# Performance work log

Measured on AMD Instinct MI355X. Metric: run time of the kernel, lower is better.

The kernel has to match this reference:

```python
import jax, jax.numpy as jnp
import numpy as np

B, T, D = 2, 2048, 1024
H, d = 16, 64
INNER = H * d
K = 4  # conv_size
EPS_RMS = 1e-6
EPS_NORM = 1e-12


def _dconv(x, w, b):
    # depthwise causal conv: x (B,T,C), w (C,K), b (C,)
    xp = jnp.pad(x, ((0, 0), (K - 1, 0), (0, 0)))
    Tt = x.shape[1]
    out = b
    for k in range(K):
        out = out + xp[:, k:k + Tt] * w[:, k]
    return out


def _l2norm(x):
    n = jnp.sqrt(jnp.sum(x * x, axis=-1, keepdims=True))
    return x / jnp.maximum(n, EPS_NORM)


def setup_inputs() -> dict:
    key = jax.random.key(0)
    ks = jax.random.split(key, 12)
    s = 0.02
    inp = {
        'x': jax.random.normal(ks[0], (B, T, D), jnp.float32),
        'Wq': jax.random.normal(ks[1], (D, INNER), jnp.float32) * s,
        'Wk': jax.random.normal(ks[2], (D, INNER), jnp.float32) * s,
        'Wv': jax.random.normal(ks[3], (D, INNER), jnp.float32) * s,
        'Wa': jax.random.normal(ks[4], (D, H), jnp.float32) * s,
        'ba': jnp.full((H,), 2.0, jnp.float32),
        'Wb': jax.random.normal(ks[5], (D, H), jnp.float32) * s,
        'bb': jnp.zeros((H,), jnp.float32),
        'Wg': jax.random.normal(ks[6], (D, INNER), jnp.float32) * s,
        'Wo': jax.random.normal(ks[7], (INNER, D), jnp.float32) * s,
        'cq_w': jax.random.normal(ks[8], (INNER, K), jnp.float32) * 0.3,
        'cq_b': jnp.zeros((INNER,), jnp.float32),
        'ck_w': jax.random.normal(ks[9], (INNER, K), jnp.float32) * 0.3,
        'ck_b': jnp.zeros((INNER,), jnp.float32),
        'cv_w': jax.random.normal(ks[10], (INNER, K), jnp.float32) * 0.3,
        'cv_b': jnp.zeros((INNER,), jnp.float32),
        'gamma': jnp.zeros((INNER,), jnp.float32),
    }
    return inp


def reference(x, Wq, Wk, Wv, Wa, ba, Wb, bb, Wg, Wo,
              cq_w, cq_b, ck_w, ck_b, cv_w, cv_b, gamma):
    q = jax.nn.silu(_dconv(x @ Wq, cq_w, cq_b))
    k = jax.nn.silu(_dconv(x @ Wk, ck_w, ck_b))
    v = jax.nn.silu(_dconv(x @ Wv, cv_w, cv_b))
    q = _l2norm(q.reshape(B, T, H, d))
    k = _l2norm(k.reshape(B, T, H, d))
    v = v.reshape(B, T, H, d)
    alpha = jax.nn.sigmoid(x @ Wa + ba)  # (B,T,H)
    beta = jax.nn.sigmoid(x @ Wb + bb)   # (B,T,H)
    gate = jax.nn.silu(x @ Wg)           # (B,T,INNER)

    I_d = jnp.eye(d, dtype=x.dtype)

    def step(S, ins):
        q_t, k_t, v_t, a_t, b_t = ins  # q/k/v: (B,H,d); a,b: (B,H)
        a = a_t[..., None, None]
        b = b_t[..., None, None]
        kkT = k_t[..., :, None] * k_t[..., None, :]   # (B,H,d,d)
        vkT = v_t[..., :, None] * k_t[..., None, :]
        decay = a * (I_d - b * kkT)
        S = jnp.matmul(S, decay) + b * vkT
        o = jnp.einsum('bhde,bhe->bhd', S, q_t)
        return S, o

    # time-major scan inputs
    qT = jnp.transpose(q, (1, 0, 2, 3))
    kT = jnp.transpose(k, (1, 0, 2, 3))
    vT = jnp.transpose(v, (1, 0, 2, 3))
    aT = jnp.transpose(alpha, (1, 0, 2))
    bT = jnp.transpose(beta, (1, 0, 2))
    S0 = jnp.zeros((B, H, d, d), x.dtype)
    _, oT = jax.lax.scan(step, S0, (qT, kT, vT, aT, bT))  # (T,B,H,d)

    out = jnp.transpose(oT, (1, 0, 2, 3)).reshape(B, T, INNER)
    rms = jnp.sqrt(jnp.mean(out * out, axis=-1, keepdims=True) + EPS_RMS)
    out = out / rms * (1.0 + gamma)
    out = out * gate
    return out @ Wo
```

## Files before the change

### kernel.cpp

```cpp
#include <hip/hip_runtime.h>
#include <hip/hip_bf16.h>
#include <cmath>

#define B_ 2
#define T_ 2048
#define D_ 1024
#define H_ 16
#define DH 64
#define INNER_ 1024
#define BT (B_*T_)
#define NCH 32
#define NU (B_*H_*NCH)

typedef __attribute__((ext_vector_type(8))) __bf16 bf16x8;
typedef __attribute__((ext_vector_type(4))) float f32x4;
typedef const __attribute__((address_space(1))) unsigned gas_u32;
typedef __attribute__((address_space(3))) unsigned las_u32;

__device__ __forceinline__ void async16(const void* g, void* l) {
  __builtin_amdgcn_global_load_lds((gas_u32*)g, (las_u32*)l, 16, 0, 0);
}

__device__ __forceinline__ ushort bfr(float x) {
  __hip_bfloat16 t = __float2bfloat16(x);
  return *(ushort*)&t;
}
__device__ __forceinline__ void st_bf4(__hip_bfloat16* p, float a, float b, float c, float d) {
  ushort4 u; u.x = bfr(a); u.y = bfr(b); u.z = bfr(c); u.w = bfr(d);
  *(ushort4*)p = u;
}

__global__ __launch_bounds__(256) void cvt_bf16_kernel(const float* __restrict__ in,
                                                       __hip_bfloat16* __restrict__ out,
                                                       int n4) {
  int i = blockIdx.x * 256 + threadIdx.x;
  if (i >= n4) return;
  float4 v = *(const float4*)(in + (size_t)i * 4);
  __hip_bfloat16 t[4];
  t[0] = __float2bfloat16(v.x); t[1] = __float2bfloat16(v.y);
  t[2] = __float2bfloat16(v.z); t[3] = __float2bfloat16(v.w);
  *(uint2*)(out + (size_t)i * 4) = *(uint2*)t;
}

__global__ __launch_bounds__(256) void transpose_cvt_kernel(const float* __restrict__ in,
                                                            __hip_bfloat16* __restrict__ out,
                                                            int R, int C) {
  __shared__ float tile[32][33];
  const int bc = blockIdx.x * 32, br = blockIdx.y * 32;
  const int tx = threadIdx.x & 31, ty = threadIdx.x >> 5;
#pragma unroll
  for (int i = 0; i < 32; i += 8)
    tile[ty + i][tx] = in[(size_t)(br + ty + i) * C + bc + tx];
  __syncthreads();
#pragma unroll
  for (int i = 0; i < 32; i += 8)
    out[(size_t)(bc + ty + i) * R + br + tx] = __float2bfloat16(tile[tx][ty + i]);
}

__global__ __launch_bounds__(256) void wab_kernel(const float* __restrict__ Wa,
                                                  const float* __restrict__ Wb,
                                                  __hip_bfloat16* __restrict__ Wabt) {
  int idx = blockIdx.x * 256 + threadIdx.x;
  int j = idx >> 10, k = idx & 1023;
  float v = 0.f;
  if (j < 16) v = Wa[k * 16 + j];
  else if (j < 32) v = Wb[k * 16 + (j - 16)];
  Wabt[idx] = __float2bfloat16(v);
}

__global__ __launch_bounds__(256) void gemm_bf16(const __hip_bfloat16* __restrict__ A,
                                                 const __hip_bfloat16* __restrict__ Bt,
                                                 float* __restrict__ C,
                                                 int M, int N, int K, int act) {
  __shared__ __hip_bfloat16 As[128 * 32];
  __shared__ __hip_bfloat16 Bs[128 * 32];
  const int tid = threadIdx.x;
  const int lane = tid & 63, wave = tid >> 6;
  const int wr = wave >> 1, wc = wave & 1;
  const int m0 = blockIdx.y * 128, n0 = blockIdx.x * 128;
  const int srow = tid >> 2, skoff = (tid & 3) * 8;
  const int l15 = lane & 15, lg = lane >> 4;

  f32x4 acc[4][4];
#pragma unroll
  for (int m = 0; m < 4; ++m)
#pragma unroll
    for (int n = 0; n < 4; ++n) acc[m][n] = (f32x4)0.f;

  char* asB = (char*)As;
  char* bsB = (char*)Bs;
  const int ldsw = wave * 1024;

  for (int k0 = 0; k0 < K; k0 += 32) {
    async16(A + (size_t)(m0 + srow) * K + k0 + skoff, asB + ldsw);
    async16(A + (size_t)(m0 + 64 + srow) * K + k0 + skoff, asB + 4096 + ldsw);
    async16(Bt + (size_t)(n0 + srow) * K + k0 + skoff, bsB + ldsw);
    async16(Bt + (size_t)(n0 + 64 + srow) * K + k0 + skoff, bsB + 4096 + ldsw);
    __syncthreads();

    bf16x8 af[4], bfg[4];
#pragma unroll
    for (int m = 0; m < 4; ++m)
      af[m] = *(const bf16x8*)(asB + ((wr * 64 + m * 16 + l15) * 32 + lg * 8) * 2);
#pragma unroll
    for (int n = 0; n < 4; ++n)
      bfg[n] = *(const bf16x8*)(bsB + ((wc * 64 + n * 16 + l15) * 32 + lg * 8) * 2);
#pragma unroll
    for (int m = 0; m < 4; ++m)
#pragma unroll
      for (int n = 0; n < 4; ++n)
        acc[m][n] = __builtin_amdgcn_mfma_f32_16x16x32_bf16(af[m], bfg[n], acc[m][n], 0, 0, 0);
    __syncthreads();
  }

#pragma unroll
  for (int m = 0; m < 4; ++m) {
    const int rbase = m0 + wr * 64 + m * 16 + lg * 4;
#pragma unroll
    for (int n = 0; n < 4; ++n) {
      const int col = n0 + wc * 64 + n * 16 + l15;
#pragma unroll
      for (int r = 0; r < 4; ++r) {
        float vv = acc[m][n][r];
        if (act == 1) vv = vv / (1.f + expf(-vv));
        C[(size_t)(rbase + r) * N + col] = vv;
      }
    }
  }
}

__global__ __launch_bounds__(256) void gemm_ab(const __hip_bfloat16* __restrict__ A,
                                               const __hip_bfloat16* __restrict__ Bt,
                                               const float* __restrict__ ba,
                                               const float* __restrict__ bb2,
                                               float* __restrict__ alpha,
                                               float* __restrict__ beta, int K) {
  __shared__ __hip_bfloat16 As[128 * 32];
  __shared__ __hip_bfloat16 Bs[128 * 32];
  const int tid = threadIdx.x;
  const int lane = tid & 63, wave = tid >> 6;
  const int wr = wave >> 1, wc = wave & 1;
  const int m0 = blockIdx.y * 128;
  const int srow = tid >> 2, skoff = (tid & 3) * 8;
  const int l15 = lane & 15, lg = lane >> 4;

  f32x4 acc[4][2];
#pragma unroll
  for (int m = 0; m < 4; ++m)
#pragma unroll
    for (int n = 0; n < 2; ++n) acc[m][n] = (f32x4)0.f;

  char* asB = (char*)As;
  char* bsB = (char*)Bs;
  const int ldsw = wave * 1024;

  for (int k0 = 0; k0 < K; k0 += 32) {
    async16(A + (size_t)(m0 + srow) * K + k0 + skoff, asB + ldsw);
    async16(A + (size_t)(m0 + 64 + srow) * K + k0 + skoff, asB + 4096 + ldsw);
    async16(Bt + (size_t)srow * K + k0 + skoff, bsB + ldsw);
    async16(Bt + (size_t)(64 + srow) * K + k0 + skoff, bsB + 4096 + ldsw);
    __syncthreads();
    if (wc == 0) {
      bf16x8 af[4], bfg[2];
#pragma unroll
      for (int m = 0; m < 4; ++m)
        af[m] = *(const bf16x8*)(asB + ((wr * 64 + m * 16 + l15) * 32 + lg * 8) * 2);
#pragma unroll
      for (int n = 0; n < 2; ++n)
        bfg[n] = *(const bf16x8*)(bsB + ((n * 16 + l15) * 32 + lg * 8) * 2);
#pragma unroll
      for (int m = 0; m < 4; ++m)
#pragma unroll
        for (int n = 0; n < 2; ++n)
          acc[m][n] = __builtin_amdgcn_mfma_f32_16x16x32_bf16(af[m], bfg[n], acc[m][n], 0, 0, 0);
    }
    __syncthreads();
  }
  if (wc != 0) return;
#pragma unroll
  for (int m = 0; m < 4; ++m) {
    const int rbase = m0 + wr * 64 + m * 16 + lg * 4;
#pragma unroll
    for (int n = 0; n < 2; ++n) {
      const int col = n * 16 + l15;
      const float bias = (n == 0) ? ba[l15] : bb2[l15];
      float* dst = (n == 0) ? alpha : beta;
#pragma unroll
      for (int r = 0; r < 4; ++r) {
        float vv = acc[m][n][r] + bias;
        dst[(size_t)(rbase + r) * H_ + l15] = 1.f / (1.f + expf(-vv));
      }
    }
  }
}

__device__ __forceinline__ bf16x8 pfrag(const __hip_bfloat16* buf, int row, int ks, int lg) {
  return *(const bf16x8*)((const char*)buf + row * 128 + ks * 64 + lg * 16);
}

__global__ __launch_bounds__(512, 2) void gemm256(const __hip_bfloat16* __restrict__ A,
                                                  const __hip_bfloat16* __restrict__ Bt,
                                                  float* __restrict__ C,
                                                  int M, int N, int K, int act) {
  __shared__ __hip_bfloat16 As[2][256 * 64];
  __shared__ __hip_bfloat16 Bs[2][256 * 64];
  const int tid = threadIdx.x;
  const int lane = tid & 63, wv = tid >> 6;
  const int wr = wv >> 2, wc = wv & 3;
  const int m0 = blockIdx.y * 256, n0 = blockIdx.x * 256;
  const int l15 = lane & 15, lg = lane >> 4;
  const int sr8 = lane >> 3, sc = (lane & 7) * 8;

  f32x4 acc[8][4];
#pragma unroll
  for (int m = 0; m < 8; ++m)
#pragma unroll
    for (int n = 0; n < 4; ++n) acc[m][n] = (f32x4)0.f;

  auto stage = [&](int kt, int bsel) {
    const size_t k0 = (size_t)kt * 64;
    const __hip_bfloat16* Ab = A + (size_t)(m0 + wv * 8 + sr8) * K + k0 + sc;
    const __hip_bfloat16* Bb = Bt + (size_t)(n0 + wv * 8 + sr8) * K + k0 + sc;
    char* al = (char*)As[bsel] + wv * 1024;
    char* bl = (char*)Bs[bsel] + wv * 1024;
#pragma unroll
    for (int q = 0; q < 4; ++q) {
      async16(Ab + (size_t)q * 64 * K, al + q * 8192);
      async16(Bb + (size_t)q * 64 * K, bl + q * 8192);
    }
  };

  const int NT = K >> 6;
  stage(0, 0);
  __syncthreads();
  int cur = 0;
  for (int kt = 0; kt < NT; ++kt) {
    if (kt + 1 < NT) stage(kt + 1, cur ^ 1);
#pragma unroll
    for (int ks = 0; ks < 2; ++ks) {
      bf16x8 af[8], bfg[4];
#pragma unroll
      for (int m = 0; m < 8; ++m)
        af[m] = pfrag(As[cur], wr * 128 + m * 16 + l15, ks, lg);
#pragma unroll
      for (int n = 0; n < 4; ++n)
        bfg[n] = pfrag(Bs[cur], wc * 64 + n * 16 + l15, ks, lg);
#pragma unroll
      for (int m = 0; m < 8; ++m)
#pragma unroll
        for (int n = 0; n < 4; ++n)
          acc[m][n] = __builtin_amdgcn_mfma_f32_16x16x32_bf16(af[m], bfg[n], acc[m][n], 0, 0, 0);
    }
    __syncthreads();
    cur ^= 1;
  }

#pragma unroll
  for (int m = 0; m < 8; ++m) {
    const int rbase = m0 + wr * 128 + m * 16 + lg * 4;
#pragma unroll
    for (int n = 0; n < 4; ++n) {
      const int col = n0 + wc * 64 + n * 16 + l15;
      if (act == 2) {
        const int which = col >> 10;
        const int ncol = col & 1023;
        float* dst = C + (size_t)which * ((size_t)BT * INNER_) +
                     (size_t)rbase * 1024 + ncol;
#pragma unroll
        for (int r = 0; r < 4; ++r) {
          float vv = acc[m][n][r];
          if (which == 3) vv = vv / (1.f + expf(-vv));
          dst[(size_t)r * 1024] = vv;
        }
      } else {
#pragma unroll
        for (int r = 0; r < 4; ++r)
          C[(size_t)(rbase + r) * N + col] = acc[m][n][r];
      }
    }
  }
}

__global__ __launch_bounds__(256) void convnorm_kernel(
    const float* __restrict__ qpre, const float* __restrict__ kpre, const float* __restrict__ vpre,
    const float* __restrict__ cqw, const float* __restrict__ cqb,
    const float* __restrict__ ckw, const float* __restrict__ ckb,
    const float* __restrict__ cvw, const float* __restrict__ cvb,
    float* __restrict__ qn, float* __restrict__ kn, float* __restrict__ vn) {
  const int bt = blockIdx.x;
  const int t = bt & (T_ - 1);
  const int tid = threadIdx.x;
  const int c = tid * 4;

  auto run = [&](const float* __restrict__ pre, const float* __restrict__ w,
                 const float* __restrict__ bias, float* __restrict__ out, bool norm) {
    float r[4];
    float4 bv = *(const float4*)(bias + c);
    r[0] = bv.x; r[1] = bv.y; r[2] = bv.z; r[3] = bv.w;
    float wl[4][4];
#pragma unroll
    for (int i = 0; i < 4; ++i) {
      float4 wv = *(const float4*)(w + (size_t)(c + i) * 4);
      wl[i][0] = wv.x; wl[i][1] = wv.y; wl[i][2] = wv.z; wl[i][3] = wv.w;
    }
#pragma unroll
    for (int kk = 0; kk < 4; ++kk) {
      int tt = t - 3 + kk;
      if (tt >= 0) {
        float4 xv = *(const float4*)(pre + (size_t)(bt - 3 + kk) * INNER_ + c);
        float xa[4] = {xv.x, xv.y, xv.z, xv.w};
#pragma unroll
        for (int i = 0; i < 4; ++i) r[i] += xa[i] * wl[i][kk];
      }
    }
#pragma unroll
    for (int i = 0; i < 4; ++i) r[i] = r[i] / (1.f + expf(-r[i]));
    if (norm) {
      float ss = r[0]*r[0] + r[1]*r[1] + r[2]*r[2] + r[3]*r[3];
      ss += __shfl_xor(ss, 1); ss += __shfl_xor(ss, 2);
      ss += __shfl_xor(ss, 4); ss += __shfl_xor(ss, 8);
      float n = sqrtf(ss);
      float sc = 1.f / fmaxf(n, 1e-12f);
#pragma unroll
      for (int i = 0; i < 4; ++i) r[i] *= sc;
    }
    float4 ov = {r[0], r[1], r[2], r[3]};
    *(float4*)(out + (size_t)bt * INNER_ + c) = ov;
  };

  run(qpre, cqw, cqb, qn, true);
  run(kpre, ckw, ckb, kn, true);
  run(vpre, cvw, cvb, vn, false);
}

#define BST 72
#define MST 65

__device__ __forceinline__ bf16x8 fragld(const __hip_bfloat16* buf, int row, int kk, int lg) {
  return *(const bf16x8*)(buf + row * BST + kk * 32 + lg * 8);
}

__global__ __launch_bounds__(256) void precomp_kernel(
    const float* __restrict__ qn, const float* __restrict__ kn, const float* __restrict__ vn,
    const float* __restrict__ alpha, const float* __restrict__ beta,
    __hip_bfloat16* __restrict__ Zg, __hip_bfloat16* __restrict__ G2g,
    float* __restrict__ AVg, float* __restrict__ G1g, float* __restrict__ P63g) {
  __shared__ __hip_bfloat16 sKb[64 * BST], sKip[64 * BST], sKipT[64 * BST];
  __shared__ __hip_bfloat16 sQp[64 * BST], sVb[64 * BST];
  __shared__ float sM[64 * MST];
  __shared__ __hip_bfloat16 sWT[64 * BST], sVtT[64 * BST], sAttn[64 * BST];
  __shared__ float sP[64], sIP[64], sBP[64], sB[64];

  const int u = blockIdx.x;
  const int bh = u >> 5, c = u & 31;
  const int b = bh >> 4, h = bh & 15;
  const int tid = threadIdx.x, lane = tid & 63, wv = tid >> 6;
  const int l15 = lane & 15, lg = lane >> 4;
  const size_t bt0 = (size_t)b * T_ + (size_t)c * 64;
  const size_t hofs = (size_t)h * DH;

  if (wv == 0) {
    float a = alpha[(bt0 + lane) * H_ + h];
    float bb = beta[(bt0 + lane) * H_ + h];
    float la = logf(a);
#pragma unroll
    for (int d = 1; d < 64; d <<= 1) {
      float y = __shfl_up(la, d);
      if (lane >= d) la += y;
    }
    float P = expf(la);
    sP[lane] = P;
    sIP[lane] = 1.f / P;
    sBP[lane] = bb * P;
    sB[lane] = bb;
    if (lane == 63) P63g[u] = P;
  }
  __syncthreads();

#pragma unroll
  for (int i = 0; i < 4; ++i) {
    int e = tid + i * 256;
    int row = e >> 4, c4 = (e & 15) * 4;
    size_t g = (bt0 + row) * INNER_ + hofs + c4;
    float4 kv = *(const float4*)(kn + g);
    float4 qv = *(const float4*)(qn + g);
    float4 vv = *(const float4*)(vn + g);
    float bp = sBP[row], ip = sIP[row], pp = sP[row], bo = sB[row];
    st_bf4(&sKb[row * BST + c4], kv.x * bp, kv.y * bp, kv.z * bp, kv.w * bp);
    st_bf4(&sKip[row * BST + c4], kv.x * ip, kv.y * ip, kv.z * ip, kv.w * ip);
    st_bf4(&sQp[row * BST + c4], qv.x * pp, qv.y * pp, qv.z * pp, qv.w * pp);
    st_bf4(&sVb[row * BST + c4], vv.x * bo, vv.y * bo, vv.z * bo, vv.w * bo);
    sKipT[(c4 + 0) * BST + row] = __float2bfloat16(kv.x * ip);
    sKipT[(c4 + 1) * BST + row] = __float2bfloat16(kv.y * ip);
    sKipT[(c4 + 2) * BST + row] = __float2bfloat16(kv.z * ip);
    sKipT[(c4 + 3) * BST + row] = __float2bfloat16(kv.w * ip);
  }
  __syncthreads();

  if (wv < 2) {
#pragma unroll
    for (int tt = wv * 2; tt < wv * 2 + 2; ++tt) {
      for (int n = 0; n <= tt; ++n) {
        f32x4 acc = (f32x4)0.f;
#pragma unroll
        for (int kk = 0; kk < 2; ++kk)
          acc = __builtin_amdgcn_mfma_f32_16x16x32_bf16(
              fragld(sKb, tt * 16 + l15, kk, lg), fragld(sKip, n * 16 + l15, kk, lg), acc, 0, 0, 0);
#pragma unroll
        for (int q = 0; q < 4; ++q) {
          int r = tt * 16 + lg * 4 + q, cl = n * 16 + l15;
          sM[r * MST + cl] = (cl < r) ? acc[q] : 0.f;
        }
      }
    }
  } else {
#pragma unroll
    for (int tt = (wv - 2) * 2; tt < (wv - 2) * 2 + 2; ++tt) {
      for (int n = 0; n < 4; ++n) {
        if (n <= tt) {
          f32x4 acc = (f32x4)0.f;
#pragma unroll
          for (int kk = 0; kk < 2; ++kk)
            acc = __builtin_amdgcn_mfma_f32_16x16x32_bf16(
                fragld(sQp, tt * 16 + l15, kk, lg), fragld(sKip, n * 16 + l15, kk, lg), acc, 0, 0, 0);
#pragma unroll
          for (int q = 0; q < 4; ++q) {
            int r = tt * 16 + lg * 4 + q, cl = n * 16 + l15;
            sAttn[r * BST + cl] = __float2bfloat16((cl <= r) ? acc[q] : 0.f);
          }
        } else {
#pragma unroll
          for (int q = 0; q < 4; ++q) {
            int r = tt * 16 + lg * 4 + q, cl = n * 16 + l15;
            sAttn[r * BST + cl] = __float2bfloat16(0.f);
          }
        }
      }
    }
  }
  __syncthreads();

  if (wv < 2) {
    const __hip_bfloat16* RHS = wv ? sVb : sKb;
    __hip_bfloat16* XT = wv ? sVtT : sWT;
    const int j = lane;
    float X[64];
#pragma unroll
    for (int t = 0; t < 64; ++t) {
      float a0 = 0.f, a1 = 0.f, a2 = 0.f, a3 = 0.f;
      int mr = __float_as_int(sM[t * MST + j]);
      int s = 0;
#pragma unroll
      for (; s + 3 < t; s += 4) {
        a0 += __int_as_float(__builtin_amdgcn_readlane(mr, s + 0)) * X[s + 0];
        a1 += __int_as_float(__builtin_amdgcn_readlane(mr, s + 1)) * X[s + 1];
        a2 += __int_as_float(__builtin_amdgcn_readlane(mr, s + 2)) * X[s + 2];
        a3 += __int_as_float(__builtin_amdgcn_readlane(mr, s + 3)) * X[s + 3];
      }
#pragma unroll
      for (; s < t; ++s)
        a0 += __int_as_float(__builtin_amdgcn_readlane(mr, s)) * X[s];
      X[t] = __bfloat162float(RHS[t * BST + j]) - ((a0 + a1) + (a2 + a3));
    }
#pragma unroll
    for (int t = 0; t < 64; t += 4)
      st_bf4(&XT[j * BST + t], X[t], X[t + 1], X[t + 2], X[t + 3]);
  }
  __syncthreads();

  const float p63 = sP[63];
  const int tt = wv;
  const size_t go = (size_t)u * 4096;
#pragma unroll
  for (int n = 0; n < 4; ++n) {
    f32x4 av = (f32x4)0.f, aw = (f32x4)0.f, g1 = (f32x4)0.f, g2 = (f32x4)0.f;
#pragma unroll
    for (int kk = 0; kk < 2; ++kk) {
      bf16x8 at = fragld(sAttn, tt * 16 + l15, kk, lg);
      bf16x8 kt = fragld(sKipT, tt * 16 + l15, kk, lg);
      bf16x8 bv = fragld(sVtT, n * 16 + l15, kk, lg);
      bf16x8 bw = fragld(sWT, n * 16 + l15, kk, lg);
      av = __builtin_amdgcn_mfma_f32_16x16x32_bf16(at, bv, av, 0, 0, 0);
      aw = __builtin_amdgcn_mfma_f32_16x16x32_bf16(at, bw, aw, 0, 0, 0);
      g1 = __builtin_amdgcn_mfma_f32_16x16x32_bf16(kt, bv, g1, 0, 0, 0);
      g2 = __builtin_amdgcn_mfma_f32_16x16x32_bf16(kt, bw, g2, 0, 0, 0);
    }
#pragma unroll
    for (int q = 0; q < 4; ++q) {
      int r = tt * 16 + lg * 4 + q, cl = n * 16 + l15;
      AVg[go + r * 64 + cl] = av[q];
      float qp = __bfloat162float(sQp[r * BST + cl]);
      Zg[go + r * 64 + cl] = __float2bfloat16(qp - aw[q]);
      G1g[go + cl * 64 + r] = p63 * g1[q];
      G2g[go + r * 64 + cl] = __float2bfloat16(p63 * g2[q]);
    }
  }
}

__device__ __forceinline__ bf16x8 sfrag(const __hip_bfloat16* buf, int row, int kk, int lg) {
  int byte = row * 128 + kk * 64 + lg * 16;
  byte ^= (row & 7) << 4;
  return *(const bf16x8*)((const char*)buf + byte);
}

__global__ __launch_bounds__(256) void chunkrec_kernel(
    const __hip_bfloat16* __restrict__ Zg, const __hip_bfloat16* __restrict__ G2g,
    const float* __restrict__ AVg, const float* __restrict__ G1g,
    const float* __restrict__ P63g, float* __restrict__ o) {
  __shared__ __align__(16) __hip_bfloat16 sR[16 * 64];
  __shared__ __align__(16) __hip_bfloat16 sZ[2][64 * 64];
  __shared__ __align__(16) __hip_bfloat16 sG2[2][64 * 64];
  const int blk = blockIdx.x;
  const int bh = blk >> 2;
  const int jb = blk & 3;
  const int b = bh >> 4, h = bh & 15;
  const int tid = threadIdx.x, lane = tid & 63, wv = tid >> 6;
  const int l15 = lane & 15, lg = lane >> 4;
  const size_t btb = (size_t)b * T_;
  const size_t hofs = (size_t)h * DH;

  f32x4 R = (f32x4)0.f;

  uint4 zr[2], gr[2];
  const int e0 = tid * 2;

  auto issue = [&](int c) {
    size_t ub = ((size_t)bh * NCH + c) * 4096;
#pragma unroll
    for (int i = 0; i < 2; ++i) {
      zr[i] = *(const uint4*)(Zg + ub + (size_t)(e0 + i) * 8);
      gr[i] = *(const uint4*)(G2g + ub + (size_t)(e0 + i) * 8);
    }
  };
  auto commit = [&](int buf) {
#pragma unroll
    for (int i = 0; i < 2; ++i) {
      int e = e0 + i;
      int row = e >> 3, colb = (e & 7) * 16;
      int byte = (row * 128 + colb) ^ ((row & 7) << 4);
      *(uint4*)((char*)sZ[buf] + byte) = zr[i];
      *(uint4*)((char*)sG2[buf] + byte) = gr[i];
    }
  };

  issue(0);
  commit(0);
  int cur = 0;
  for (int c = 0; c < NCH; ++c) {
#pragma unroll
    for (int q = 0; q < 4; ++q) {
      int i = lg * 4 + q;
      int byte = (i * 128 + (wv * 16 + l15) * 2) ^ ((i & 7) << 4);
      *(__hip_bfloat16*)((char*)sR + byte) = __float2bfloat16(R[q]);
    }
    __syncthreads();

    const size_t ub = ((size_t)bh * NCH + c) * 4096;
    float avr[4], g1r[4];
#pragma unroll
    for (int q = 0; q < 4; ++q) {
      int t = wv * 16 + lg * 4 + q;
      avr[q] = AVg[ub + t * 64 + jb * 16 + l15];
      g1r[q] = G1g[ub + (jb * 16 + lg * 4 + q) * 64 + wv * 16 + l15];
    }
    float p63 = P63g[(size_t)bh * NCH + c];
    if (c + 1 < NCH) issue(c + 1);

    bf16x8 zA[2], rF[2], gB[2];
#pragma unroll
    for (int kk = 0; kk < 2; ++kk) {
      zA[kk] = sfrag(sZ[cur], wv * 16 + l15, kk, lg);
      rF[kk] = sfrag(sR, l15, kk, lg);
      gB[kk] = sfrag(sG2[cur], wv * 16 + l15, kk, lg);
    }
    f32x4 oacc = (f32x4)0.f, gacc = (f32x4)0.f;
#pragma unroll
    for (int kk = 0; kk < 2; ++kk) {
      oacc = __builtin_amdgcn_mfma_f32_16x16x32_bf16(zA[kk], rF[kk], oacc, 0, 0, 0);
      gacc = __builtin_amdgcn_mfma_f32_16x16x32_bf16(rF[kk], gB[kk], gacc, 0, 0, 0);
    }
#pragma unroll
    for (int q = 0; q < 4; ++q) {
      int t = wv * 16 + lg * 4 + q;
      o[(btb + (size_t)c * 64 + t) * INNER_ + hofs + jb * 16 + l15] = avr[q] + oacc[q];
      R[q] = p63 * R[q] + g1r[q] - gacc[q];
    }
    __syncthreads();
    if (c + 1 < NCH) commit(cur ^ 1);
    cur ^= 1;
  }
}

__global__ __launch_bounds__(256) void rmsgate_kernel(const float* __restrict__ o,
    const float* __restrict__ gate, const float* __restrict__ gamma,
    __hip_bfloat16* __restrict__ outn) {
  const int bt = blockIdx.x;
  const int tid = threadIdx.x;
  const size_t base = (size_t)bt * INNER_ + tid * 4;
  float4 ov = *(const float4*)(o + base);
  float ss = ov.x*ov.x + ov.y*ov.y + ov.z*ov.z + ov.w*ov.w;
#pragma unroll
  for (int m = 1; m <= 32; m <<= 1) ss += __shfl_xor(ss, m);
  __shared__ float red[4];
  if ((tid & 63) == 0) red[tid >> 6] = ss;
  __syncthreads();
  float tot = red[0] + red[1] + red[2] + red[3];
  float rms = sqrtf(tot * (1.f / (float)INNER_) + 1e-6f);
  float inv = 1.f / rms;
  float4 gm = *(const float4*)(gamma + tid * 4);
  float4 gt = *(const float4*)(gate + base);
  __hip_bfloat16 t[4];
  t[0] = __float2bfloat16(ov.x * inv * (1.f + gm.x) * gt.x);
  t[1] = __float2bfloat16(ov.y * inv * (1.f + gm.y) * gt.y);
  t[2] = __float2bfloat16(ov.z * inv * (1.f + gm.z) * gt.z);
  t[3] = __float2bfloat16(ov.w * inv * (1.f + gm.w) * gt.w);
  *(uint2*)(outn + base) = *(uint2*)t;
}

extern "C" void kernel_launch(void* const* d_in, const int* in_sizes, int n_in,
                              void* d_out, int out_size, void* d_ws, size_t ws_size,
                              hipStream_t stream) {
  const float* x   = (const float*)d_in[0];
  const float* Wq  = (const float*)d_in[1];
  const float* Wk  = (const float*)d_in[2];
  const float* Wv  = (const float*)d_in[3];
  const float* Wa  = (const float*)d_in[4];
  const float* ba  = (const float*)d_in[5];
  const float* Wb  = (const float*)d_in[6];
  const float* bb  = (const float*)d_in[7];
  const float* Wg  = (const float*)d_in[8];
  const float* Wo  = (const float*)d_in[9];
  const float* cqw = (const float*)d_in[10];
  const float* cqb = (const float*)d_in[11];
  const float* ckw = (const float*)d_in[12];
  const float* ckb = (const float*)d_in[13];
  const float* cvw = (const float*)d_in[14];
  const float* cvb = (const float*)d_in[15];
  const float* gamma = (const float*)d_in[16];

  float* ws = (float*)d_ws;
  const size_t N1 = (size_t)BT * INNER_;
  float* qpre = ws;
  float* kpre = ws + N1;
  float* vpre = ws + 2 * N1;
  float* gate = ws + 3 * N1;
  float* qn   = ws + 4 * N1;
  float* kn   = ws + 5 * N1;
  float* vn   = ws + 6 * N1;
  float* alpha = ws + 7 * N1;
  float* beta  = alpha + (size_t)BT * H_;
  __hip_bfloat16* wt0 = (__hip_bfloat16*)(beta + (size_t)BT * H_);
  __hip_bfloat16* Wot = wt0 + 4 * (size_t)D_ * INNER_;
  float* P63s = (float*)(Wot + (size_t)D_ * INNER_);
  __hip_bfloat16* Wabt = (__hip_bfloat16*)(P63s + NU);
  __hip_bfloat16* xb  = (__hip_bfloat16*)vn;
  float* AVg = qpre;
  __hip_bfloat16* Zg  = (__hip_bfloat16*)kpre;
  __hip_bfloat16* G2g = Zg + (size_t)NU * 4096;
  float* G1g = vpre;
  float* obuf = qn;
  __hip_bfloat16* nrmb = (__hip_bfloat16*)kn;
  float* outp = (float*)d_out;

  cvt_bf16_kernel<<<(BT * D_ / 4 + 255) / 256, 256, 0, stream>>>(x, xb, BT * D_ / 4);
  dim3 tgrid(INNER_ / 32, D_ / 32);
  transpose_cvt_kernel<<<tgrid, 256, 0, stream>>>(Wq, wt0, D_, INNER_);
  transpose_cvt_kernel<<<tgrid, 256, 0, stream>>>(Wk, wt0 + (size_t)D_ * INNER_, D_, INNER_);
  transpose_cvt_kernel<<<tgrid, 256, 0, stream>>>(Wv, wt0 + 2 * (size_t)D_ * INNER_, D_, INNER_);
  transpose_cvt_kernel<<<tgrid, 256, 0, stream>>>(Wg, wt0 + 3 * (size_t)D_ * INNER_, D_, INNER_);
  transpose_cvt_kernel<<<dim3(D_ / 32, INNER_ / 32), 256, 0, stream>>>(Wo, Wot, INNER_, D_);
  wab_kernel<<<(128 * 1024) / 256, 256, 0, stream>>>(Wa, Wb, Wabt);

  gemm256<<<dim3(4 * INNER_ / 256, BT / 256), 512, 0, stream>>>(
      xb, wt0, qpre, BT, 4 * INNER_, D_, 2);
  gemm_ab<<<dim3(1, BT / 128), 256, 0, stream>>>(xb, Wabt, ba, bb, alpha, beta, D_);

  convnorm_kernel<<<BT, 256, 0, stream>>>(qpre, kpre, vpre, cqw, cqb, ckw, ckb,
                                          cvw, cvb, qn, kn, vn);

  precomp_kernel<<<NU, 256, 0, stream>>>(qn, kn, vn, alpha, beta, Zg, G2g, AVg, G1g, P63s);
  chunkrec_kernel<<<B_ * H_ * 4, 256, 0, stream>>>(Zg, G2g, AVg, G1g, P63s, obuf);

  rmsgate_kernel<<<BT, 256, 0, stream>>>(obuf, gate, gamma, nrmb);
  gemm_bf16<<<dim3(D_ / 128, BT / 128), 256, 0, stream>>>(nrmb, Wot, outp, BT, D_, INNER_, 0);
}
```

Baseline: 409.4 us.

## Blocked triangular solve with MFMA in precomp, reuse gemm256 for output projection

After: 371.0 us. 1.1x faster.

```diff
diff --git a/kernel.cpp b/kernel.cpp
--- a/kernel.cpp
+++ b/kernel.cpp
@@ -66,67 +66,6 @@
   if (j < 16) v = Wa[k * 16 + j];
   else if (j < 32) v = Wb[k * 16 + (j - 16)];
   Wabt[idx] = __float2bfloat16(v);
-}
-
-__global__ __launch_bounds__(256) void gemm_bf16(const __hip_bfloat16* __restrict__ A,
-                                                 const __hip_bfloat16* __restrict__ Bt,
-                                                 float* __restrict__ C,
-                                                 int M, int N, int K, int act) {
-  __shared__ __hip_bfloat16 As[128 * 32];
-  __shared__ __hip_bfloat16 Bs[128 * 32];
-  const int tid = threadIdx.x;
-  const int lane = tid & 63, wave = tid >> 6;
-  const int wr = wave >> 1, wc = wave & 1;
-  const int m0 = blockIdx.y * 128, n0 = blockIdx.x * 128;
-  const int srow = tid >> 2, skoff = (tid & 3) * 8;
-  const int l15 = lane & 15, lg = lane >> 4;
-
-  f32x4 acc[4][4];
-#pragma unroll
-  for (int m = 0; m < 4; ++m)
-#pragma unroll
-    for (int n = 0; n < 4; ++n) acc[m][n] = (f32x4)0.f;
-
-  char* asB = (char*)As;
-  char* bsB = (char*)Bs;
-  const int ldsw = wave * 1024;
-
-  for (int k0 = 0; k0 < K; k0 += 32) {
-    async16(A + (size_t)(m0 + srow) * K + k0 + skoff, asB + ldsw);
-    async16(A + (size_t)(m0 + 64 + srow) * K + k0 + skoff, asB + 4096 + ldsw);
-    async16(Bt + (size_t)(n0 + srow) * K + k0 + skoff, bsB + ldsw);
-    async16(Bt + (size_t)(n0 + 64 + srow) * K + k0 + skoff, bsB + 4096 + ldsw);
-    __syncthreads();
-
-    bf16x8 af[4], bfg[4];
-#pragma unroll
-    for (int m = 0; m < 4; ++m)
-      af[m] = *(const bf16x8*)(asB + ((wr * 64 + m * 16 + l15) * 32 + lg * 8) * 2);
-#pragma unroll
-    for (int n = 0; n < 4; ++n)
-      bfg[n] = *(const bf16x8*)(bsB + ((wc * 64 + n * 16 + l15) * 32 + lg * 8) * 2);
-#pragma unroll
-    for (int m = 0; m < 4; ++m)
-#pragma unroll
-      for (int n = 0; n < 4; ++n)
-        acc[m][n] = __builtin_amdgcn_mfma_f32_16x16x32_bf16(af[m], bfg[n], acc[m][n], 0, 0, 0);
-    __syncthreads();
-  }
-
-#pragma unroll
-  for (int m = 0; m < 4; ++m) {
-    const int rbase = m0 + wr * 64 + m * 16 + lg * 4;
-#pragma unroll
-    for (int n = 0; n < 4; ++n) {
-      const int col = n0 + wc * 64 + n * 16 + l15;
-#pragma unroll
-      for (int r = 0; r < 4; ++r) {
-        float vv = acc[m][n][r];
-        if (act == 1) vv = vv / (1.f + expf(-vv));
-        C[(size_t)(rbase + r) * N + col] = vv;
-      }
-    }
-  }
 }
 
 __global__ __launch_bounds__(256) void gemm_ab(const __hip_bfloat16* __restrict__ A,
@@ -182,7 +121,6 @@
     const int rbase = m0 + wr * 64 + m * 16 + lg * 4;
 #pragma unroll
     for (int n = 0; n < 2; ++n) {
-      const int col = n * 16 + l15;
       const float bias = (n == 0) ? ba[l15] : bb2[l15];
       float* dst = (n == 0) ? alpha : beta;
 #pragma unroll
@@ -334,21 +272,21 @@
 }
 
 #define BST 72
-#define MST 65
 
 __device__ __forceinline__ bf16x8 fragld(const __hip_bfloat16* buf, int row, int kk, int lg) {
   return *(const bf16x8*)(buf + row * BST + kk * 32 + lg * 8);
 }
 
-__global__ __launch_bounds__(256) void precomp_kernel(
+__global__ __launch_bounds__(256, 2) void precomp_kernel(
     const float* __restrict__ qn, const float* __restrict__ kn, const float* __restrict__ vn,
     const float* __restrict__ alpha, const float* __restrict__ beta,
     __hip_bfloat16* __restrict__ Zg, __hip_bfloat16* __restrict__ G2g,
     float* __restrict__ AVg, float* __restrict__ G1g, float* __restrict__ P63g) {
   __shared__ __hip_bfloat16 sKb[64 * BST], sKip[64 * BST], sKipT[64 * BST];
-  __shared__ __hip_bfloat16 sQp[64 * BST], sVb[64 * BST];
-  __shared__ float sM[64 * MST];
-  __shared__ __hip_bfloat16 sWT[64 * BST], sVtT[64 * BST], sAttn[64 * BST];
+  __shared__ __hip_bfloat16 sQp[64 * BST], sAttn[64 * BST];
+  __shared__ __hip_bfloat16 sXT[128 * BST];
+  __shared__ __hip_bfloat16 sM[64 * BST];
+  __shared__ float sMd[4][16][16];
   __shared__ float sP[64], sIP[64], sBP[64], sB[64];
 
   const int u = blockIdx.x;
@@ -389,11 +327,18 @@
     st_bf4(&sKb[row * BST + c4], kv.x * bp, kv.y * bp, kv.z * bp, kv.w * bp);
     st_bf4(&sKip[row * BST + c4], kv.x * ip, kv.y * ip, kv.z * ip, kv.w * ip);
     st_bf4(&sQp[row * BST + c4], qv.x * pp, qv.y * pp, qv.z * pp, qv.w * pp);
-    st_bf4(&sVb[row * BST + c4], vv.x * bo, vv.y * bo, vv.z * bo, vv.w * bo);
     sKipT[(c4 + 0) * BST + row] = __float2bfloat16(kv.x * ip);
     sKipT[(c4 + 1) * BST + row] = __float2bfloat16(kv.y * ip);
     sKipT[(c4 + 2) * BST + row] = __float2bfloat16(kv.z * ip);
     sKipT[(c4 + 3) * BST + row] = __float2bfloat16(kv.w * ip);
+    sXT[(c4 + 0) * BST + row] = __float2bfloat16(kv.x * bp);
+    sXT[(c4 + 1) * BST + row] = __float2bfloat16(kv.y * bp);
+    sXT[(c4 + 2) * BST + row] = __float2bfloat16(kv.z * bp);
+    sXT[(c4 + 3) * BST + row] = __float2bfloat16(kv.w * bp);
+    sXT[(64 + c4 + 0) * BST + row] = __float2bfloat16(vv.x * bo);
+    sXT[(64 + c4 + 1) * BST + row] = __float2bfloat16(vv.y * bo);
+    sXT[(64 + c4 + 2) * BST + row] = __float2bfloat16(vv.z * bo);
+    sXT[(64 + c4 + 3) * BST + row] = __float2bfloat16(vv.w * bo);
   }
   __syncthreads();
 
@@ -406,10 +351,17 @@
         for (int kk = 0; kk < 2; ++kk)
           acc = __builtin_amdgcn_mfma_f32_16x16x32_bf16(
               fragld(sKb, tt * 16 + l15, kk, lg), fragld(sKip, n * 16 + l15, kk, lg), acc, 0, 0, 0);
-#pragma unroll
-        for (int q = 0; q < 4; ++q) {
-          int r = tt * 16 + lg * 4 + q, cl = n * 16 + l15;
-          sM[r * MST + cl] = (cl < r) ? acc[q] : 0.f;
+        if (n < tt) {
+#pragma unroll
+          for (int q = 0; q < 4; ++q)
+            sM[(tt * 16 + lg * 4 + q) * BST + n * 16 + l15] = __float2bfloat16(acc[q]);
+        } else {
+#pragma unroll
+          for (int q = 0; q < 4; ++q) {
+            int rr = lg * 4 + q;
+            sMd[tt][rr][l15] = (l15 < rr) ? acc[q] : 0.f;
+            sM[(tt * 16 + rr) * BST + tt * 16 + l15] = __float2bfloat16(0.f);
+          }
         }
       }
     }
@@ -430,43 +382,53 @@
           }
         } else {
 #pragma unroll
-          for (int q = 0; q < 4; ++q) {
-            int r = tt * 16 + lg * 4 + q, cl = n * 16 + l15;
-            sAttn[r * BST + cl] = __float2bfloat16(0.f);
-          }
+          for (int q = 0; q < 4; ++q)
+            sAttn[(tt * 16 + lg * 4 + q) * BST + n * 16 + l15] = __float2bfloat16(0.f);
         }
       }
     }
   }
   __syncthreads();
 
-  if (wv < 2) {
-    const __hip_bfloat16* RHS = wv ? sVb : sKb;
-    __hip_bfloat16* XT = wv ? sVtT : sWT;
-    const int j = lane;
-    float X[64];
-#pragma unroll
-    for (int t = 0; t < 64; ++t) {
-      float a0 = 0.f, a1 = 0.f, a2 = 0.f, a3 = 0.f;
-      int mr = __float_as_int(sM[t * MST + j]);
-      int s = 0;
-#pragma unroll
-      for (; s + 3 < t; s += 4) {
-        a0 += __int_as_float(__builtin_amdgcn_readlane(mr, s + 0)) * X[s + 0];
-        a1 += __int_as_float(__builtin_amdgcn_readlane(mr, s + 1)) * X[s + 1];
-        a2 += __int_as_float(__builtin_amdgcn_readlane(mr, s + 2)) * X[s + 2];
-        a3 += __int_as_float(__builtin_amdgcn_readlane(mr, s + 3)) * X[s + 3];
+  auto diag_solve = [&](int I) {
+    if (wv < 2) {
+      const int cc = wv * 64 + lane;
+      float x[16];
+#pragma unroll
+      for (int t = 0; t < 16; ++t) {
+        float r = __bfloat162float(sXT[cc * BST + I * 16 + t]);
+#pragma unroll
+        for (int s = 0; s < t; ++s) r -= sMd[I][t][s] * x[s];
+        x[t] = r;
+        sXT[cc * BST + I * 16 + t] = __float2bfloat16(r);
       }
-#pragma unroll
-      for (; s < t; ++s)
-        a0 += __int_as_float(__builtin_amdgcn_readlane(mr, s)) * X[s];
-      X[t] = __bfloat162float(RHS[t * BST + j]) - ((a0 + a1) + (a2 + a3));
-    }
-#pragma unroll
-    for (int t = 0; t < 64; t += 4)
-      st_bf4(&XT[j * BST + t], X[t], X[t + 1], X[t + 2], X[t + 3]);
-  }
+    }
+  };
+
+  diag_solve(0);
   __syncthreads();
+#pragma unroll
+  for (int I = 1; I < 4; ++I) {
+    const int KK = (I == 3) ? 2 : 1;
+#pragma unroll
+    for (int ct2 = 0; ct2 < 2; ++ct2) {
+      const int ct = wv * 2 + ct2;
+      f32x4 uacc = (f32x4)0.f;
+#pragma unroll
+      for (int kk = 0; kk < KK; ++kk)
+        uacc = __builtin_amdgcn_mfma_f32_16x16x32_bf16(
+            fragld(sXT, ct * 16 + l15, kk, lg), fragld(sM, I * 16 + l15, kk, lg), uacc, 0, 0, 0);
+#pragma unroll
+      for (int q = 0; q < 4; ++q) {
+        const int cc = ct * 16 + lg * 4 + q, t = I * 16 + l15;
+        float old = __bfloat162float(sXT[cc * BST + t]);
+        sXT[cc * BST + t] = __float2bfloat16(old - uacc[q]);
+      }
+    }
+    __syncthreads();
+    diag_solve(I);
+    __syncthreads();
+  }
 
   const float p63 = sP[63];
   const int tt = wv;
@@ -478,8 +440,8 @@
     for (int kk = 0; kk < 2; ++kk) {
       bf16x8 at = fragld(sAttn, tt * 16 + l15, kk, lg);
       bf16x8 kt = fragld(sKipT, tt * 16 + l15, kk, lg);
-      bf16x8 bv = fragld(sVtT, n * 16 + l15, kk, lg);
-      bf16x8 bw = fragld(sWT, n * 16 + l15, kk, lg);
+      bf16x8 bv = fragld(sXT, 64 + n * 16 + l15, kk, lg);
+      bf16x8 bw = fragld(sXT, n * 16 + l15, kk, lg);
       av = __builtin_amdgcn_mfma_f32_16x16x32_bf16(at, bv, av, 0, 0, 0);
       aw = __builtin_amdgcn_mfma_f32_16x16x32_bf16(at, bw, aw, 0, 0, 0);
       g1 = __builtin_amdgcn_mfma_f32_16x16x32_bf16(kt, bv, g1, 0, 0, 0);
@@ -682,5 +644,6 @@
   chunkrec_kernel<<<B_ * H_ * 4, 256, 0, stream>>>(Zg, G2g, AVg, G1g, P63s, obuf);
 
   rmsgate_kernel<<<BT, 256, 0, stream>>>(obuf, gate, gamma, nrmb);
-  gemm_bf16<<<dim3(D_ / 128, BT / 128), 256, 0, stream>>>(nrmb, Wot, outp, BT, D_, INNER_, 0);
-}
+
+  gemm256<<<dim3(D_ / 256, BT / 256), 512, 0, stream>>>(nrmb, Wot, outp, BT, D_, INNER_, 0);
+}
```
